# Performance work log

Hardware: AMD Instinct MI355X
Metric: run time of the kernel (lower is better)

## Reference

```python
import jax, jax.numpy as jnp
import numpy as np

N_HEADS = 16


def setup_inputs() -> dict:
    key = jax.random.key(0)
    ks = jax.random.split(key, 8)
    B, S, D = 4, 2048, 1024
    scale = 1.0 / np.sqrt(D)
    return {
        "x": jax.random.normal(ks[0], (B, S, D), dtype=jnp.float32),
        "Wq": jax.random.normal(ks[1], (D, D), dtype=jnp.float32) * scale,
        "bq": jax.random.normal(ks[2], (D,), dtype=jnp.float32) * 0.01,
        "Wk": jax.random.normal(ks[3], (D, D), dtype=jnp.float32) * scale,
        "bk": jax.random.normal(ks[4], (D,), dtype=jnp.float32) * 0.01,
        "Wv": jax.random.normal(ks[5], (D, D), dtype=jnp.float32) * scale,
        "bv": jax.random.normal(ks[6], (D,), dtype=jnp.float32) * 0.01,
        "mask": jax.random.randint(ks[7], (B, S), 0, 2, dtype=jnp.int32),
    }


def reference(x, Wq, bq, Wk, bk, Wv, bv, mask):
    B, S, D = x.shape
    H = N_HEADS
    W = D // H
    # QKV projections (Linear with weight stored input-major: y = x @ W + b)
    q = (x @ Wq + bq).reshape(B, S, H, W).transpose(0, 2, 1, 3)  # (B,H,S,W)
    k = (x @ Wk + bk).reshape(B, S, H, W).transpose(0, 2, 1, 3)
    v = (x @ Wv + bv).reshape(B, S, H, W).transpose(0, 2, 1, 3)
    # scaled dot-product scores: (B,H,S,S)
    scores = jnp.einsum("bhsw,bhtw->bhst", q, k) / jnp.sqrt(jnp.asarray(W, x.dtype))
    # mask==1 means masked (subtract large constant), per original code
    scores = scores - 10000.0 * mask[:, None, None, :].astype(x.dtype)
    attn = jax.nn.softmax(scores, axis=-1)  # dropout p=0 -> identity
    h = jnp.einsum("bhst,bhtw->bhsw", attn, v)  # (B,H,S,W)
    h = h.transpose(0, 2, 1, 3).reshape(B, S, D)
    return h
```

## Files before the change

kernel.cpp:

```cpp
#include <hip/hip_runtime.h>
#include <math.h>

#define B_NUM 4
#define S_LEN 2048
#define D_DIM 1024
#define H_NUM 16
#define W_DIM 64

typedef float4 f4;
typedef _Float16 f16;
typedef f16 f16x8 __attribute__((ext_vector_type(8)));
typedef f16 f16x4 __attribute__((ext_vector_type(4)));
typedef float floatx4 __attribute__((ext_vector_type(4)));

#define GLOAD_LDS16(gp, lp)                                                     \
    __builtin_amdgcn_global_load_lds(                                           \
        (const __attribute__((address_space(1))) void*)(gp),                    \
        (__attribute__((address_space(3))) void*)(lp), 16, 0, 0)

#define TR_BLOCKS   768
#define CAST_BLOCKS 8192

__global__ __launch_bounds__(256) void prep_kernel(
    const int* __restrict__ mask, short* __restrict__ fwdmap,
    int* __restrict__ cnt,
    const float* __restrict__ Wq, const float* __restrict__ Wk,
    const float* __restrict__ Wv, f16* __restrict__ wt16,
    const float* __restrict__ x, f16* __restrict__ x16)
{
    __shared__ __align__(16) char smraw[64 * 68 * 4];
    const int bx  = blockIdx.x;
    const int tid = threadIdx.x;

    if (bx < 4) {
        int* sc = (int*)smraw;
        const int b  = bx;
        const int t0 = tid * 8;
#pragma unroll
        for (int j = 0; j < 8; ++j) fwdmap[b * S_LEN + t0 + j] = 0;
        int kept[8], c = 0;
#pragma unroll
        for (int j = 0; j < 8; ++j) {
            kept[j] = (mask[b * S_LEN + t0 + j] == 0);
            c += kept[j];
        }
        sc[tid] = c;
        __syncthreads();
        for (int off = 1; off < 256; off <<= 1) {
            int add = (tid >= off) ? sc[tid - off] : 0;
            __syncthreads();
            sc[tid] += add;
            __syncthreads();
        }
        int base = sc[tid] - c;
#pragma unroll
        for (int j = 0; j < 8; ++j)
            if (kept[j]) fwdmap[b * S_LEN + (base++)] = (short)(t0 + j);
        if (tid == 255) {
            cnt[b * 4 + 0] = sc[255];
            cnt[b * 4 + 1] = (sc[255] + 63) & ~63;
            cnt[b * 4 + 2] = (sc[255] + 127) & ~127;
            cnt[b * 4 + 3] = (sc[255] + 255) & ~255;
        }
    } else if (bx < 4 + TR_BLOCKS) {
        float (*ts)[68] = (float(*)[68])smraw;
        const int idx = bx - 4;
        const int k0 = (idx & 15) * 64;
        const int n0 = ((idx >> 4) & 15) * 64;
        const int z  = idx >> 8;
        const float* Wsel = (z == 0) ? Wq : (z == 1) ? Wk : Wv;
        f16* outp = wt16 + (size_t)z * D_DIM * D_DIM;

        const int r  = tid >> 4;
        const int c4 = (tid & 15) * 4;
#pragma unroll
        for (int i = 0; i < 4; ++i) {
            f4 t = *(const f4*)&Wsel[(size_t)(k0 + r + i * 16) * D_DIM + n0 + c4];
            *(f4*)&ts[r + i * 16][c4] = t;
        }
        __syncthreads();
#pragma unroll
        for (int i = 0; i < 4; ++i) {
            int id2 = tid + i * 256;
            int nl = id2 >> 4;
            int k4 = (id2 & 15) * 4;
            f16x4 o;
#pragma unroll
            for (int j = 0; j < 4; ++j) o[j] = (f16)ts[k4 + j][nl];
            *(f16x4*)&outp[(size_t)(n0 + nl) * D_DIM + k0 + k4] = o;
        }
    } else {
        const size_t i = (size_t)(bx - 4 - TR_BLOCKS) * 256 + tid;
        f4 t = *(const f4*)&x[i * 4];
        f16x4 o;
        o[0] = (f16)t.x; o[1] = (f16)t.y; o[2] = (f16)t.z; o[3] = (f16)t.w;
        *(f16x4*)&x16[i * 4] = o;
    }
}

#define QSTAGE(BUF, K0) do {                                                    \
    _Pragma("unroll") for (int it_ = 0; it_ < 4; ++it_) {                       \
        int chunk_ = wid * 4 + it_;                                             \
        GLOAD_LDS16(&x16[(size_t)arows[it_] * D_DIM + (K0) + scw],              \
                    &As[BUF][chunk_ * 512]);                                    \
        GLOAD_LDS16(&Bg[(size_t)(chunk_ * 8 + srow) * D_DIM + (K0) + scw],      \
                    &Bs[BUF][chunk_ * 512]);                                    \
    } } while (0)

#define QCOMPUTE(BUF) do {                                                      \
    _Pragma("unroll") for (int kh_ = 0; kh_ < 2; ++kh_) {                       \
        const int csw_ = ((kh_ * 4 + quad) ^ (lx & 7)) * 8;                     \
        f16x8 af_[4], bf_[4];                                                   \
        _Pragma("unroll") for (int tm_ = 0; tm_ < 4; ++tm_)                     \
            af_[tm_] = *(const f16x8*)&As[BUF][(wm * 64 + tm_ * 16 + lx) * 64 + csw_]; \
        _Pragma("unroll") for (int tn_ = 0; tn_ < 4; ++tn_)                     \
            bf_[tn_] = *(const f16x8*)&Bs[BUF][(wn * 64 + tn_ * 16 + lx) * 64 + csw_]; \
        _Pragma("unroll") for (int tm_ = 0; tm_ < 4; ++tm_)                     \
        _Pragma("unroll") for (int tn_ = 0; tn_ < 4; ++tn_)                     \
            acc[tm_][tn_] = __builtin_amdgcn_mfma_f32_16x16x32_f16(             \
                af_[tm_], bf_[tn_], acc[tm_][tn_], 0, 0, 0);                    \
    } } while (0)

#define QVM0BAR() do {                                                          \
    asm volatile("s_waitcnt vmcnt(0)" ::: "memory");                            \
    __builtin_amdgcn_s_barrier();                                               \
    } while (0)

__global__ __launch_bounds__(256) void qkv_mfma_kernel(
    const f16* __restrict__ x16, const f16* __restrict__ wt16,
    const float* __restrict__ bq, const float* __restrict__ bk,
    const float* __restrict__ bv, const short* __restrict__ fwdmap,
    const int* __restrict__ cnt,
    f16* __restrict__ Qo, f16* __restrict__ Ko, f16* __restrict__ Vo)
{
    __shared__ f16 As[2][128 * 64];
    __shared__ f16 Bs[2][128 * 64];

    const int tid  = threadIdx.x;
    const int lane = tid & 63;
    const int wid  = tid >> 6;
    const int lx   = lane & 15;
    const int quad = lane >> 4;
    const int wm   = wid >> 1;
    const int wn   = wid & 1;

    const int r0    = blockIdx.y * 128;
    const int nt    = blockIdx.x;
    const int midx  = nt >> 3;
    const int c0    = (nt & 7) * 128;
    const int bB    = r0 >> 11;
    const int r0loc = r0 & (S_LEN - 1);

    if (midx > 0 && r0loc >= cnt[bB * 4 + 2]) return;

    const f16* Bg = wt16 + (size_t)midx * D_DIM * D_DIM + (size_t)c0 * D_DIM;

    const int srow = lane >> 3;
    const int scw  = ((lane & 7) ^ srow) * 8;

    int arows[4];
#pragma unroll
    for (int it = 0; it < 4; ++it) {
        int rl = (wid * 4 + it) * 8 + srow;
        arows[it] = (midx == 0)
            ? (r0 + rl)
            : (bB * S_LEN + (int)fwdmap[bB * S_LEN + r0loc + rl]);
    }

    floatx4 acc[4][4];
#pragma unroll
    for (int a = 0; a < 4; ++a)
#pragma unroll
        for (int b = 0; b < 4; ++b) { acc[a][b][0]=0.f; acc[a][b][1]=0.f; acc[a][b][2]=0.f; acc[a][b][3]=0.f; }

    QSTAGE(0, 0);
    QVM0BAR();

#pragma unroll 2
    for (int t = 0; t < 14; t += 2) {
        QSTAGE(1, (t + 1) * 64);
        QCOMPUTE(0);
        QVM0BAR();
        QSTAGE(0, (t + 2) * 64);
        QCOMPUTE(1);
        QVM0BAR();
    }
    QSTAGE(1, 15 * 64);
    QCOMPUTE(0);
    QVM0BAR();
    QCOMPUTE(1);

    const float* bp = (midx == 0) ? bq : (midx == 1) ? bk : bv;
    float bias[4];
#pragma unroll
    for (int tn = 0; tn < 4; ++tn)
        bias[tn] = bp[c0 + wn * 64 + tn * 16 + lx];

    if (midx == 0) {
#pragma unroll
        for (int tm = 0; tm < 4; ++tm) {
            int s = r0loc + wm * 64 + tm * 16 + quad * 4;
#pragma unroll
            for (int tn = 0; tn < 4; ++tn) {
                int gc = c0 + wn * 64 + tn * 16 + lx;
                int h = gc >> 6, w = gc & 63;
                size_t base = (((size_t)(bB * H_NUM + h)) * S_LEN + s) * W_DIM + w;
#pragma unroll
                for (int rr = 0; rr < 4; ++rr)
                    Qo[base + (size_t)rr * W_DIM] =
                        (f16)((acc[tm][tn][rr] + bias[tn]) * 0.125f);
            }
        }
    } else if (midx == 1) {
#pragma unroll
        for (int tm = 0; tm < 4; ++tm) {
            int jc = r0loc + wm * 64 + tm * 16 + quad * 4;
#pragma unroll
            for (int tn = 0; tn < 4; ++tn) {
                int gc = c0 + wn * 64 + tn * 16 + lx;
                int h = gc >> 6, w = gc & 63;
                size_t base = (((size_t)(bB * H_NUM + h)) * S_LEN + jc) * W_DIM + w;
#pragma unroll
                for (int rr = 0; rr < 4; ++rr)
                    Ko[base + (size_t)rr * W_DIM] = (f16)(acc[tm][tn][rr] + bias[tn]);
            }
        }
    } else {
#pragma unroll
        for (int tm = 0; tm < 4; ++tm) {
            int jc = r0loc + wm * 64 + tm * 16 + quad * 4;
#pragma unroll
            for (int tn = 0; tn < 4; ++tn) {
                int gc = c0 + wn * 64 + tn * 16 + lx;
                int h = gc >> 6, w = gc & 63;
                f16x4 v;
#pragma unroll
                for (int rr = 0; rr < 4; ++rr) v[rr] = (f16)(acc[tm][tn][rr] + bias[tn]);
                *(f16x4*)&Vo[(((size_t)(bB * H_NUM + h)) * W_DIM + w) * S_LEN + jc] = v;
            }
        }
    }
}

#define LSTR 72

__global__ __launch_bounds__(256) void attn_kernel(
    const f16* __restrict__ Q, const f16* __restrict__ Kc,
    const f16* __restrict__ Vct, const int* __restrict__ cnt,
    float* __restrict__ out)
{
    __shared__ f16 Ks[64][LSTR];
    __shared__ f16 Vs[64][LSTR];

    const int tid  = threadIdx.x;
    const int lane = tid & 63;
    const int wid  = tid >> 6;
    const int lx   = lane & 15;
    const int quad = lane >> 4;
    const int qt = blockIdx.x, h = blockIdx.y, bb = blockIdx.z;

    const int count = cnt[bb * 4 + 0];
    const int scp   = cnt[bb * 4 + 1];

    const size_t hoff = ((size_t)(bb * H_NUM + h)) * S_LEN * W_DIM;
    const f16* Qg = Q + hoff + (size_t)qt * 128 * W_DIM;
    const f16* Kg = Kc + hoff;
    const f16* Vg = Vct + hoff;

    f16x8 qb[2][2];
#pragma unroll
    for (int u = 0; u < 2; ++u) {
        int qrow = u * 64 + wid * 16 + lx;
        qb[u][0] = *(const f16x8*)&Qg[(size_t)qrow * W_DIM + quad * 8];
        qb[u][1] = *(const f16x8*)&Qg[(size_t)qrow * W_DIM + 32 + quad * 8];
    }

    floatx4 o[2][4];
    float lsum[2] = {0.f, 0.f};
#pragma unroll
    for (int u = 0; u < 2; ++u)
#pragma unroll
        for (int wb = 0; wb < 4; ++wb) { o[u][wb][0]=0.f; o[u][wb][1]=0.f; o[u][wb][2]=0.f; o[u][wb][3]=0.f; }

    for (int k0 = 0; k0 < scp; k0 += 64) {
        __syncthreads();
#pragma unroll
        for (int it = 0; it < 2; ++it) {
            int idx = tid + it * 256;
            int row = idx >> 3, c8 = (idx & 7) * 8;
            *(f16x8*)&Ks[row][c8] = *(const f16x8*)&Kg[(size_t)(k0 + row) * W_DIM + c8];
            *(f16x8*)&Vs[row][c8] = *(const f16x8*)&Vg[(size_t)row * S_LEN + k0 + c8];
        }
        __syncthreads();

        const bool tail = (k0 + 64 > count);

        f16x4 pb[2][4];
#pragma unroll
        for (int n = 0; n < 4; ++n) {
            f16x8 ka0 = *(const f16x8*)&Ks[n * 16 + lx][quad * 8];
            f16x8 ka1 = *(const f16x8*)&Ks[n * 16 + lx][32 + quad * 8];
            const int kb = k0 + n * 16 + quad * 4;
#pragma unroll
            for (int u = 0; u < 2; ++u) {
                floatx4 s; s[0]=0.f; s[1]=0.f; s[2]=0.f; s[3]=0.f;
                s = __builtin_amdgcn_mfma_f32_16x16x32_f16(ka0, qb[u][0], s, 0, 0, 0);
                s = __builtin_amdgcn_mfma_f32_16x16x32_f16(ka1, qb[u][1], s, 0, 0, 0);
                float p[4], ls = 0.f;
                if (tail) {
#pragma unroll
                    for (int r = 0; r < 4; ++r) {
                        float sv = (kb + r < count) ? s[r] : -1.0e4f;
                        p[r] = __expf(sv); ls += p[r];
                    }
                } else {
#pragma unroll
                    for (int r = 0; r < 4; ++r) { p[r] = __expf(s[r]); ls += p[r]; }
                }
                lsum[u] += ls;
#pragma unroll
                for (int r = 0; r < 4; ++r) pb[u][n][r] = (f16)p[r];
            }
        }

#pragma unroll
        for (int wb = 0; wb < 4; ++wb) {
#pragma unroll
            for (int n = 0; n < 4; ++n) {
                f16x4 va = *(const f16x4*)&Vs[wb * 16 + lx][n * 16 + quad * 4];
#pragma unroll
                for (int u = 0; u < 2; ++u)
                    o[u][wb] = __builtin_amdgcn_mfma_f32_16x16x16f16(va, pb[u][n], o[u][wb], 0, 0, 0);
            }
        }
    }

#pragma unroll
    for (int u = 0; u < 2; ++u) {
        float ls = lsum[u];
        ls += __shfl_xor(ls, 16);
        ls += __shfl_xor(ls, 32);
        const float rl = 1.0f / ls;
        const int q = qt * 128 + u * 64 + wid * 16 + lx;
        const size_t base = ((size_t)bb * S_LEN + q) * D_DIM + h * W_DIM;
#pragma unroll
        for (int wb = 0; wb < 4; ++wb) {
            f4 r;
            r.x = o[u][wb][0] * rl;
            r.y = o[u][wb][1] * rl;
            r.z = o[u][wb][2] * rl;
            r.w = o[u][wb][3] * rl;
            *(f4*)&out[base + wb * 16 + quad * 4] = r;
        }
    }
}

extern "C" void kernel_launch(void* const* d_in, const int* in_sizes, int n_in,
                              void* d_out, int out_size, void* d_ws, size_t ws_size,
                              hipStream_t stream)
{
    const float* x    = (const float*)d_in[0];
    const float* Wq   = (const float*)d_in[1];
    const float* bq   = (const float*)d_in[2];
    const float* Wk   = (const float*)d_in[3];
    const float* bk   = (const float*)d_in[4];
    const float* Wv   = (const float*)d_in[5];
    const float* bv   = (const float*)d_in[6];
    const int*   mask = (const int*)d_in[7];
    float* out = (float*)d_out;

    const size_t per = (size_t)B_NUM * H_NUM * S_LEN * W_DIM;
    f16*   Q      = (f16*)d_ws;
    f16*   Kc     = Q + per;
    f16*   Vct    = Kc + per;
    f16*   x16    = Vct + per;
    f16*   wt16   = x16 + (size_t)(B_NUM * S_LEN) * D_DIM;
    int*   cnt    = (int*)(wt16 + (size_t)3 * D_DIM * D_DIM);
    short* fwdmap = (short*)(cnt + 4 * B_NUM);

    prep_kernel<<<4 + TR_BLOCKS + CAST_BLOCKS, 256, 0, stream>>>(
        mask, fwdmap, cnt, Wq, Wk, Wv, wt16, x, x16);
    qkv_mfma_kernel<<<dim3(24, 64), 256, 0, stream>>>(
        x16, wt16, bq, bk, bv, fwdmap, cnt, Q, Kc, Vct);
    attn_kernel<<<dim3(S_LEN / 128, H_NUM, B_NUM), 256, 0, stream>>>(
        Q, Kc, Vct, cnt, out);
}
```

Baseline: 216.5 us.

## Use 16x16x32 MFMA for PV with permuted K rows and XOR-swizzled LDS

The PV product moves from 16x16x16 to 16x16x32 f16 MFMA, halving the instruction count and LDS reads for V. K rows are loaded into shared memory in a permuted key order, so the score outputs of two adjacent 16-key MFMA tiles form one 8-wide B operand. The padded LDS stride is replaced by an XOR swizzle on 16-byte chunks to avoid bank conflicts without padding. The key-index mapping used for tail masking must match the permutation exactly, which adds correctness risk.

Measured after the change: 219.0 us. No clear change (+1.1%).

```diff
diff --git a/kernel.cpp b/kernel.cpp
--- a/kernel.cpp
+++ b/kernel.cpp
@@ -242,15 +242,13 @@
     }
 }
 
-#define LSTR 72
-
 __global__ __launch_bounds__(256) void attn_kernel(
     const f16* __restrict__ Q, const f16* __restrict__ Kc,
     const f16* __restrict__ Vct, const int* __restrict__ cnt,
     float* __restrict__ out)
 {
-    __shared__ f16 Ks[64][LSTR];
-    __shared__ f16 Vs[64][LSTR];
+    __shared__ f16 Ks[64][64];
+    __shared__ f16 Vs[64][64];
 
     const int tid  = threadIdx.x;
     const int lane = tid & 63;
@@ -282,25 +280,31 @@
 #pragma unroll
         for (int wb = 0; wb < 4; ++wb) { o[u][wb][0]=0.f; o[u][wb][1]=0.f; o[u][wb][2]=0.f; o[u][wb][3]=0.f; }
 
+    const int swz = lx & 7;
+
     for (int k0 = 0; k0 < scp; k0 += 64) {
         __syncthreads();
 #pragma unroll
         for (int it = 0; it < 2; ++it) {
             int idx = tid + it * 256;
-            int row = idx >> 3, c8 = (idx & 7) * 8;
-            *(f16x8*)&Ks[row][c8] = *(const f16x8*)&Kg[(size_t)(k0 + row) * W_DIM + c8];
-            *(f16x8*)&Vs[row][c8] = *(const f16x8*)&Vg[(size_t)row * S_LEN + k0 + c8];
+            int row = idx >> 3;
+            int ci  = idx & 7;
+            int cs  = (ci ^ (row & 7)) * 8;
+            int key = ((row >> 5) << 5) | (((row >> 2) & 3) << 3)
+                    | (((row >> 4) & 1) << 2) | (row & 3);
+            *(f16x8*)&Ks[row][cs] = *(const f16x8*)&Kg[(size_t)(k0 + key) * W_DIM + ci * 8];
+            *(f16x8*)&Vs[row][cs] = *(const f16x8*)&Vg[(size_t)row * S_LEN + k0 + ci * 8];
         }
         __syncthreads();
 
         const bool tail = (k0 + 64 > count);
 
-        f16x4 pb[2][4];
+        f16x8 pb8[2][2];
 #pragma unroll
         for (int n = 0; n < 4; ++n) {
-            f16x8 ka0 = *(const f16x8*)&Ks[n * 16 + lx][quad * 8];
-            f16x8 ka1 = *(const f16x8*)&Ks[n * 16 + lx][32 + quad * 8];
-            const int kb = k0 + n * 16 + quad * 4;
+            f16x8 ka0 = *(const f16x8*)&Ks[n * 16 + lx][((0 + quad) ^ swz) * 8];
+            f16x8 ka1 = *(const f16x8*)&Ks[n * 16 + lx][((4 + quad) ^ swz) * 8];
+            const int kb = k0 + ((n >> 1) << 5) + (quad << 3) + ((n & 1) << 2);
 #pragma unroll
             for (int u = 0; u < 2; ++u) {
                 floatx4 s; s[0]=0.f; s[1]=0.f; s[2]=0.f; s[3]=0.f;
@@ -319,18 +323,20 @@
                 }
                 lsum[u] += ls;
 #pragma unroll
-                for (int r = 0; r < 4; ++r) pb[u][n][r] = (f16)p[r];
+                for (int r = 0; r < 4; ++r)
+                    pb8[u][n >> 1][(n & 1) * 4 + r] = (f16)p[r];
             }
         }
 
 #pragma unroll
         for (int wb = 0; wb < 4; ++wb) {
 #pragma unroll
-            for (int n = 0; n < 4; ++n) {
-                f16x4 va = *(const f16x4*)&Vs[wb * 16 + lx][n * 16 + quad * 4];
+            for (int m = 0; m < 2; ++m) {
+                f16x8 va = *(const f16x8*)&Vs[wb * 16 + lx][((m * 4 + quad) ^ swz) * 8];
 #pragma unroll
                 for (int u = 0; u < 2; ++u)
-                    o[u][wb] = __builtin_amdgcn_mfma_f32_16x16x16f16(va, pb[u][n], o[u][wb], 0, 0, 0);
+                    o[u][wb] = __builtin_amdgcn_mfma_f32_16x16x32_f16(
+                        va, pb8[u][m], o[u][wb], 0, 0, 0);
             }
         }
     }
```

## Double-buffer attention K/V tiles with direct global-to-LDS loads and swizzle

Applied to the files above, without the earlier changes.

Rewrites the attention inner loop to prefetch the next 64-key K/V tile into a second LDS buffer with global_load_lds while the current tile is being computed, using one barrier per tile. The LDS layout drops the padded stride in favor of an XOR swizzle, and K rows are permuted so the PV product can use 16x16x32 MFMAs with 8-wide P fragments in place of 16x16x16 ones. This is meant to hide global load latency and halve the number of PV MFMA instructions. In exchange it doubles LDS usage and relies on the key permutation matching the tail-mask index arithmetic.

Result: no change. 218.7 us (+1.0%).

```diff
diff --git a/kernel.cpp b/kernel.cpp
--- a/kernel.cpp
+++ b/kernel.cpp
@@ -242,15 +242,61 @@
     }
 }
 
-#define LSTR 72
+#define ASTAGE(BUF, K0) do {                                                    \
+    _Pragma("unroll") for (int it_ = 0; it_ < 2; ++it_) {                       \
+        int idx_ = tid + it_ * 256;                                             \
+        int row_ = idx_ >> 3, ci_ = idx_ & 7;                                   \
+        int sc_  = (ci_ ^ (row_ & 7)) * 8;                                      \
+        int key_ = ((row_ >> 5) << 5) | (((row_ >> 2) & 3) << 3)                \
+                 | (((row_ >> 4) & 1) << 2) | (row_ & 3);                       \
+        GLOAD_LDS16(&Kg[(size_t)((K0) + key_) * W_DIM + sc_],                   \
+                    (f16*)Ks[BUF] + idx_ * 8);                                  \
+        GLOAD_LDS16(&Vg[(size_t)row_ * S_LEN + (K0) + sc_],                     \
+                    (f16*)Vs[BUF] + idx_ * 8);                                  \
+    } } while (0)
+
+#define ACOMPUTE(BUF, K0) do {                                                  \
+    const bool tail_ = ((K0) + 64 > count);                                     \
+    f16x8 pb8[2][2];                                                            \
+    _Pragma("unroll") for (int n = 0; n < 4; ++n) {                             \
+        f16x8 ka0 = *(const f16x8*)&Ks[BUF][n * 16 + lx][((0 + quad) ^ swz) * 8]; \
+        f16x8 ka1 = *(const f16x8*)&Ks[BUF][n * 16 + lx][((4 + quad) ^ swz) * 8]; \
+        const int kb = (K0) + ((n >> 1) << 5) + (quad << 3) + ((n & 1) << 2);   \
+        _Pragma("unroll") for (int u = 0; u < 2; ++u) {                         \
+            floatx4 s; s[0]=0.f; s[1]=0.f; s[2]=0.f; s[3]=0.f;                  \
+            s = __builtin_amdgcn_mfma_f32_16x16x32_f16(ka0, qb[u][0], s, 0, 0, 0); \
+            s = __builtin_amdgcn_mfma_f32_16x16x32_f16(ka1, qb[u][1], s, 0, 0, 0); \
+            float p[4], ls = 0.f;                                               \
+            if (tail_) {                                                        \
+                _Pragma("unroll") for (int r = 0; r < 4; ++r) {                 \
+                    float sv = (kb + r < count) ? s[r] : -1.0e4f;               \
+                    p[r] = __expf(sv); ls += p[r];                              \
+                }                                                               \
+            } else {                                                            \
+                _Pragma("unroll") for (int r = 0; r < 4; ++r) {                 \
+                    p[r] = __expf(s[r]); ls += p[r]; }                          \
+            }                                                                   \
+            lsum[u] += ls;                                                      \
+            _Pragma("unroll") for (int r = 0; r < 4; ++r)                       \
+                pb8[u][n >> 1][(n & 1) * 4 + r] = (f16)p[r];                    \
+        }                                                                       \
+    }                                                                           \
+    _Pragma("unroll") for (int wb = 0; wb < 4; ++wb) {                          \
+        _Pragma("unroll") for (int m = 0; m < 2; ++m) {                         \
+            f16x8 va = *(const f16x8*)&Vs[BUF][wb * 16 + lx][((m * 4 + quad) ^ swz) * 8]; \
+            _Pragma("unroll") for (int u = 0; u < 2; ++u)                       \
+                o[u][wb] = __builtin_amdgcn_mfma_f32_16x16x32_f16(              \
+                    va, pb8[u][m], o[u][wb], 0, 0, 0);                          \
+        }                                                                       \
+    } } while (0)
 
 __global__ __launch_bounds__(256) void attn_kernel(
     const f16* __restrict__ Q, const f16* __restrict__ Kc,
     const f16* __restrict__ Vct, const int* __restrict__ cnt,
     float* __restrict__ out)
 {
-    __shared__ f16 Ks[64][LSTR];
-    __shared__ f16 Vs[64][LSTR];
+    __shared__ f16 Ks[2][64][64];
+    __shared__ f16 Vs[2][64][64];
 
     const int tid  = threadIdx.x;
     const int lane = tid & 63;
@@ -261,6 +307,7 @@
 
     const int count = cnt[bb * 4 + 0];
     const int scp   = cnt[bb * 4 + 1];
+    const int ntile = scp >> 6;
 
     const size_t hoff = ((size_t)(bb * H_NUM + h)) * S_LEN * W_DIM;
     const f16* Qg = Q + hoff + (size_t)qt * 128 * W_DIM;
@@ -282,56 +329,22 @@
 #pragma unroll
         for (int wb = 0; wb < 4; ++wb) { o[u][wb][0]=0.f; o[u][wb][1]=0.f; o[u][wb][2]=0.f; o[u][wb][3]=0.f; }
 
-    for (int k0 = 0; k0 < scp; k0 += 64) {
-        __syncthreads();
-#pragma unroll
-        for (int it = 0; it < 2; ++it) {
-            int idx = tid + it * 256;
-            int row = idx >> 3, c8 = (idx & 7) * 8;
-            *(f16x8*)&Ks[row][c8] = *(const f16x8*)&Kg[(size_t)(k0 + row) * W_DIM + c8];
-            *(f16x8*)&Vs[row][c8] = *(const f16x8*)&Vg[(size_t)row * S_LEN + k0 + c8];
-        }
-        __syncthreads();
-
-        const bool tail = (k0 + 64 > count);
-
-        f16x4 pb[2][4];
-#pragma unroll
-        for (int n = 0; n < 4; ++n) {
-            f16x8 ka0 = *(const f16x8*)&Ks[n * 16 + lx][quad * 8];
-            f16x8 ka1 = *(const f16x8*)&Ks[n * 16 + lx][32 + quad * 8];
-            const int kb = k0 + n * 16 + quad * 4;
-#pragma unroll
-            for (int u = 0; u < 2; ++u) {
-                floatx4 s; s[0]=0.f; s[1]=0.f; s[2]=0.f; s[3]=0.f;
-                s = __builtin_amdgcn_mfma_f32_16x16x32_f16(ka0, qb[u][0], s, 0, 0, 0);
-                s = __builtin_amdgcn_mfma_f32_16x16x32_f16(ka1, qb[u][1], s, 0, 0, 0);
-                float p[4], ls = 0.f;
-                if (tail) {
-#pragma unroll
-                    for (int r = 0; r < 4; ++r) {
-                        float sv = (kb + r < count) ? s[r] : -1.0e4f;
-                        p[r] = __expf(sv); ls += p[r];
-                    }
-                } else {
-#pragma unroll
-                    for (int r = 0; r < 4; ++r) { p[r] = __expf(s[r]); ls += p[r]; }
-                }
-                lsum[u] += ls;
-#pragma unroll
-                for (int r = 0; r < 4; ++r) pb[u][n][r] = (f16)p[r];
-            }
-        }
-
-#pragma unroll
-        for (int wb = 0; wb < 4; ++wb) {
-#pragma unroll
-            for (int n = 0; n < 4; ++n) {
-                f16x4 va = *(const f16x4*)&Vs[wb * 16 + lx][n * 16 + quad * 4];
-#pragma unroll
-                for (int u = 0; u < 2; ++u)
-                    o[u][wb] = __builtin_amdgcn_mfma_f32_16x16x16f16(va, pb[u][n], o[u][wb], 0, 0, 0);
-            }
+    const int swz = lx & 7;
+
+    ASTAGE(0, 0);
+    asm volatile("s_waitcnt vmcnt(0)" ::: "memory");
+    __builtin_amdgcn_s_barrier();
+
+    for (int t = 0; t < ntile; t += 2) {
+        if (t + 1 < ntile) ASTAGE(1, (t + 1) * 64);
+        ACOMPUTE(0, t * 64);
+        asm volatile("s_waitcnt vmcnt(0)" ::: "memory");
+        __builtin_amdgcn_s_barrier();
+        if (t + 1 < ntile) {
+            if (t + 2 < ntile) ASTAGE(0, (t + 2) * 64);
+            ACOMPUTE(1, (t + 1) * 64);
+            asm volatile("s_waitcnt vmcnt(0)" ::: "memory");
+            __builtin_amdgcn_s_barrier();
         }
     }
 
```
